# Kernel optimization log

Measured on AMD Instinct MI355X. Metric: run time of the kernel, lower is better.

The kernel has to match this reference:

```python
import jax, jax.numpy as jnp
import numpy as np


def _conv1x1(x, w, b):
    # x: [B, Cin, H, W], w: [Cout, Cin], b: [Cout]
    return jnp.einsum('bchw,oc->bohw', x, w) + b[None, :, None, None]


def setup_inputs() -> dict:
    key = jax.random.key(0)
    ks = jax.random.split(key, 9)
    B, C, H, W = 32, 512, 32, 32
    Cout, dn = 512, 512
    s_in = 1.0 / np.sqrt(C)
    s_out = 1.0 / np.sqrt(Cout)
    return {
        'x': jax.random.normal(ks[0], (B, C, H, W), jnp.float32),
        'wA': jax.random.uniform(ks[1], (Cout, C), jnp.float32, -s_in, s_in),
        'bA': jax.random.uniform(ks[2], (Cout,), jnp.float32, -s_in, s_in),
        'wB': jax.random.uniform(ks[3], (dn, C), jnp.float32, -s_in, s_in),
        'bB': jax.random.uniform(ks[4], (dn,), jnp.float32, -s_in, s_in),
        'wV': jax.random.uniform(ks[5], (dn, C), jnp.float32, -s_in, s_in),
        'bV': jax.random.uniform(ks[6], (dn,), jnp.float32, -s_in, s_in),
        'wR': jax.random.uniform(ks[7], (Cout, Cout), jnp.float32, -s_out, s_out),
        'bR': jax.random.uniform(ks[8], (Cout,), jnp.float32, -s_out, s_out),
    }


def reference(x, wA, bA, wB, bB, wV, bV, wR, bR):
    Bsz, C, H, W = x.shape
    Cout = wA.shape[0]
    A = _conv1x1(x, wA, bA).reshape(Bsz, Cout, H * W)          # [B, Cout, N]
    Bm = _conv1x1(x, wB, bB).reshape(Bsz, wB.shape[0], H * W)  # [B, dn, N]
    Vm = _conv1x1(x, wV, bV).reshape(Bsz, wV.shape[0], H * W)  # [B, dn, N]
    attn_maps = jax.nn.softmax(Bm, axis=-1)                    # softmax over spatial
    attn_vectors = jax.nn.softmax(Vm, axis=-1)                 # softmax over spatial
    glob_desc = jnp.einsum('bcn,bdn->bcd', A, attn_maps)       # [B, Cout, dn]
    Z = jnp.einsum('bcd,bdn->bcn', glob_desc, attn_vectors)    # [B, Cout, N]
    Z = Z.reshape(Bsz, Cout, H, W)
    Z = _conv1x1(Z, wR, bR)
    return Z
```

## Files before the change

### kernel.cpp

```cpp
#include <hip/hip_runtime.h>
#include <stdint.h>

typedef unsigned short u16;
typedef __bf16  bf16x8 __attribute__((ext_vector_type(8)));
typedef float   f32x4  __attribute__((ext_vector_type(4)));

__device__ __forceinline__ u16 f2bf(float f) {
    union { float f; unsigned u; } c; c.f = f;
    unsigned r = c.u + 0x7fffu + ((c.u >> 16) & 1u);
    return (u16)(r >> 16);
}
__device__ __forceinline__ float bf2f(u16 b) {
    union { unsigned u; float f; } c; c.u = ((unsigned)b) << 16; return c.f;
}

__device__ __forceinline__ void g2l16(const u16* g, u16* l) {
    __builtin_amdgcn_global_load_lds(
        (__attribute__((address_space(1))) void*)(uintptr_t)g,
        (__attribute__((address_space(3))) void*)(uint32_t)(uintptr_t)l,
        16, 0, 0);
}

template <int TM, bool HAS_BIAS, bool OUT_F32, bool EPI>
__device__ __forceinline__ void gemm_core(
    const u16* __restrict__ Ab, const u16* __restrict__ Bb, void* __restrict__ C,
    const float* __restrict__ bias, int N, int K, long cbase, int m0, int n0,
    const float* __restrict__ svec, const float* __restrict__ wRbA)
{
    constexpr int MI = TM / 32;
    constexpr int NA = TM / 32;
    __shared__ __align__(16) u16 As[TM * 64];
    __shared__ __align__(16) u16 Bs[128 * 64];

    const int t = threadIdx.x;
    const int w = t >> 6, lane = t & 63;
    const int wr = w >> 1, wc = w & 1;

    f32x4 acc[MI][4];
    const f32x4 zero = {0.f, 0.f, 0.f, 0.f};
#pragma unroll
    for (int i = 0; i < MI; ++i)
#pragma unroll
        for (int j = 0; j < 4; ++j) acc[i][j] = zero;

    int  aslot[NA]; long aoff[NA];
#pragma unroll
    for (int i = 0; i < NA; ++i) {
        const int s   = i * 256 + t;
        const int row = s >> 3;
        const int col = ((s & 7) ^ (row & 7)) * 8;
        aslot[i] = s * 8;
        aoff[i]  = (long)(m0 + row) * K + col;
    }
    int  bslot[4]; long boff[4];
#pragma unroll
    for (int i = 0; i < 4; ++i) {
        const int s   = i * 256 + t;
        const int row = s >> 3;
        const int col = ((s & 7) ^ (row & 7)) * 8;
        bslot[i] = s * 8;
        boff[i]  = (long)(n0 + row) * K + col;
    }

    const int fr = lane & 15;
    const int q  = lane >> 4;
    const int o0 = ((q ^ (fr & 7)) * 8);
    const u16* fa = &As[(wr * (TM / 2) + fr) * 64];
    const u16* fb = &Bs[(wc * 64 + fr) * 64];

    for (int k0 = 0; k0 < K; k0 += 64) {
#pragma unroll
        for (int i = 0; i < NA; ++i) g2l16(Ab + aoff[i] + k0, &As[aslot[i]]);
#pragma unroll
        for (int i = 0; i < 4; ++i)  g2l16(Bb + boff[i] + k0, &Bs[bslot[i]]);
        __syncthreads();

#pragma unroll
        for (int kh = 0; kh < 2; ++kh) {
            const int o = o0 ^ (kh * 32);
            bf16x8 af[MI], bv[4];
#pragma unroll
            for (int mi = 0; mi < MI; ++mi) af[mi] = *(const bf16x8*)(fa + mi * 1024 + o);
#pragma unroll
            for (int ni = 0; ni < 4; ++ni)  bv[ni] = *(const bf16x8*)(fb + ni * 1024 + o);
#pragma unroll
            for (int mi = 0; mi < MI; ++mi)
#pragma unroll
                for (int ni = 0; ni < 4; ++ni)
                    acc[mi][ni] = __builtin_amdgcn_mfma_f32_16x16x32_bf16(
                        af[mi], bv[ni], acc[mi][ni], 0, 0, 0);
        }
        __syncthreads();
    }

    const int ccol  = n0 + wc * 64 + fr;
    const int crow0 = m0 + wr * (TM / 2) + (lane >> 4) * 4;
    float se[4];
    if (EPI) {
#pragma unroll
        for (int ni = 0; ni < 4; ++ni) se[ni] = svec[ccol + ni * 16];
    }
#pragma unroll
    for (int mi = 0; mi < MI; ++mi) {
#pragma unroll
        for (int r = 0; r < 4; ++r) {
            const int row = crow0 + mi * 16 + r;
            float add = HAS_BIAS ? bias[row] : 0.f;
            float rk  = EPI ? wRbA[row] : 0.f;
#pragma unroll
            for (int ni = 0; ni < 4; ++ni) {
                float v = acc[mi][ni][r] + add;
                if (EPI) v += rk * se[ni];
                const long idx = cbase + (long)row * N + ccol + ni * 16;
                if (OUT_F32) ((float*)C)[idx] = v;
                else         ((u16*)C)[idx]   = f2bf(v);
            }
        }
    }
}

template <int TM, bool HAS_BIAS, bool OUT_F32>
__global__ __launch_bounds__(256) void gemm_nt(
    const u16* __restrict__ A, const u16* __restrict__ B, void* __restrict__ C,
    const float* __restrict__ bias, int N, int K, long sA, long sB, long sC)
{
    const int bz = blockIdx.z;
    gemm_core<TM, HAS_BIAS, OUT_F32, false>(
        A + (long)bz * sA, B + (long)bz * sB, C, bias, N, K,
        (long)bz * sC, blockIdx.y * TM, blockIdx.x * 128, nullptr, nullptr);
}

template <int TM, bool HAS_BIAS, bool OUT_F32, bool EPI>
__global__ __launch_bounds__(256) void gemm_nt_swz(
    const u16* __restrict__ A, const u16* __restrict__ B, void* __restrict__ C,
    const float* __restrict__ bias, int N, int K, long sA, long sB, long sC,
    int bxn, int bpb, const float* __restrict__ s_all,
    const float* __restrict__ wRbA)
{
    const int blk  = blockIdx.x;
    const int xcd  = blk & 7;
    const int slot = blk >> 3;
    const int b    = xcd + 8 * (slot / bpb);
    const int wi   = slot % bpb;
    const int bx   = wi % bxn;
    const int by   = wi / bxn;
    gemm_core<TM, HAS_BIAS, OUT_F32, EPI>(
        A + (long)b * sA, B + (long)b * sB, C, bias, N, K,
        (long)b * sC, by * TM, bx * 128,
        EPI ? s_all + (long)b * 1024 : nullptr, wRbA);
}

__global__ __launch_bounds__(512) void gemm2_y(
    const u16* __restrict__ A,
    const u16* __restrict__ B,
    u16* __restrict__ C,
    const float* __restrict__ bias)
{
    constexpr int K    = 512;
    constexpr int NT   = K / 32;
    constexpr int AREG = 256 * 32;
    constexpr int BUFQ = 2 * AREG;
    __shared__ __align__(16) u16 lds[4 * BUFQ];

    const int bz = blockIdx.z;
    const int m0 = blockIdx.y * 256;
    const int n0 = blockIdx.x * 256;
    const u16* Ab = A;
    const u16* Bb = B + (long)bz * (1024 * 512);
    u16*       Cb = C + (long)bz * ((long)1536 * 1024);

    const int t    = threadIdx.x;
    const int w    = t >> 6, lane = t & 63;
    const int wr   = w >> 2, wc = w & 3;
    const int fr   = lane & 15, q = lane >> 4;

    int  aslot[2]; long agoff[2], bgoff[2];
#pragma unroll
    for (int i = 0; i < 2; ++i) {
        const int ci  = i * 512 + t;
        const int row = ci >> 2;
        const int gc  = (ci & 3) ^ ((row >> 1) & 3);
        aslot[i] = ci * 8;
        agoff[i] = (long)(m0 + row) * K + gc * 8;
        bgoff[i] = (long)(n0 + row) * K + gc * 8;
    }

    const int rchunk = (q ^ ((fr >> 1) & 3)) * 8;
    const int abase  = (wr * 128 + fr) * 32 + rchunk;
    const int bbase  = (wc * 64  + fr) * 32 + rchunk;

    f32x4 acc[8][4];
    const f32x4 zero = {0.f, 0.f, 0.f, 0.f};
#pragma unroll
    for (int i = 0; i < 8; ++i)
#pragma unroll
        for (int j = 0; j < 4; ++j) acc[i][j] = zero;

#pragma unroll
    for (int i = 0; i < 2; ++i) g2l16(Ab + agoff[i],        &lds[aslot[i]]);
#pragma unroll
    for (int i = 0; i < 2; ++i) g2l16(Bb + bgoff[i],        &lds[AREG + aslot[i]]);
#pragma unroll
    for (int i = 0; i < 2; ++i) g2l16(Ab + agoff[i] + 32,   &lds[BUFQ + aslot[i]]);
#pragma unroll
    for (int i = 0; i < 2; ++i) g2l16(Bb + bgoff[i] + 32,   &lds[BUFQ + AREG + aslot[i]]);
    asm volatile("s_waitcnt vmcnt(4)" ::: "memory");
    __builtin_amdgcn_s_barrier();
    asm volatile("" ::: "memory");

#pragma unroll
    for (int kt = 0; kt < NT; ++kt) {
        const u16* Abuf = &lds[(kt & 3) * BUFQ];
        const u16* Bbuf = Abuf + AREG;
        u16* dst = &lds[((kt + 2) & 3) * BUFQ];
        const long kg = (long)(kt + 2) * 32;

        bf16x8 av[8], bv[4];
#pragma unroll
        for (int mi = 0; mi < 8; ++mi) av[mi] = *(const bf16x8*)(Abuf + abase + mi * 512);
#pragma unroll
        for (int ni = 0; ni < 4; ++ni) bv[ni] = *(const bf16x8*)(Bbuf + bbase + ni * 512);
        if (kt + 2 < NT) {
#pragma unroll
            for (int i = 0; i < 2; ++i) g2l16(Ab + agoff[i] + kg, dst + aslot[i]);
#pragma unroll
            for (int i = 0; i < 2; ++i) g2l16(Bb + bgoff[i] + kg, dst + AREG + aslot[i]);
        }
#pragma unroll
        for (int mi = 0; mi < 8; ++mi)
#pragma unroll
            for (int ni = 0; ni < 4; ++ni)
                acc[mi][ni] = __builtin_amdgcn_mfma_f32_16x16x32_bf16(
                    av[mi], bv[ni], acc[mi][ni], 0, 0, 0);

        if (kt + 1 < NT) {
            if (kt + 2 < NT) asm volatile("s_waitcnt vmcnt(4)" ::: "memory");
            else             asm volatile("s_waitcnt vmcnt(0)" ::: "memory");
            __builtin_amdgcn_s_barrier();
            asm volatile("" ::: "memory");
        }
    }

    const int ccol  = n0 + wc * 64 + fr;
    const int crow0 = m0 + wr * 128 + q * 4;
#pragma unroll
    for (int mi = 0; mi < 8; ++mi) {
#pragma unroll
        for (int r = 0; r < 4; ++r) {
            const int row = crow0 + mi * 16 + r;
            const float add = bias[row];
#pragma unroll
            for (int ni = 0; ni < 4; ++ni)
                Cb[(long)row * 1024 + ccol + ni * 16] = f2bf(acc[mi][ni][r] + add);
        }
    }
}

__global__ __launch_bounds__(256) void cast_transpose_x(
    const float* __restrict__ in, u16* __restrict__ out)
{
    __shared__ u16 tile[64][68];
    const int bz = blockIdx.z;
    const float* ip = in  + (long)bz * (512 * 1024);
    u16*         op = out + (long)bz * (1024 * 512);
    const int c0 = blockIdx.x * 64;
    const int r0 = blockIdx.y * 64;
    const int tx = threadIdx.x & 15;
    const int ty = threadIdx.x >> 4;
#pragma unroll
    for (int p = 0; p < 4; ++p) {
        const int row = ty + 16 * p;
        float4 v = *(const float4*)(ip + (long)(r0 + row) * 1024 + c0 + 4 * tx);
        ushort4 o;
        o.x = f2bf(v.x); o.y = f2bf(v.y); o.z = f2bf(v.z); o.w = f2bf(v.w);
        *(ushort4*)&tile[row][4 * tx] = o;
    }
    __syncthreads();
#pragma unroll
    for (int p = 0; p < 4; ++p) {
        const int orow = ty + 16 * p;
        ushort4 o;
        o.x = tile[4 * tx + 0][orow];
        o.y = tile[4 * tx + 1][orow];
        o.z = tile[4 * tx + 2][orow];
        o.w = tile[4 * tx + 3][orow];
        *(ushort4*)&op[(long)(c0 + orow) * 512 + r0 + 4 * tx] = o;
    }
}

__global__ __launch_bounds__(256) void transpose_colsum(
    const u16* __restrict__ in, u16* __restrict__ out, float* __restrict__ s,
    long sIn, long sOut)
{
    __shared__ u16 tile[64][68];
    const int bz = blockIdx.z;
    const u16* ip = in  + (long)bz * sIn;
    u16*       op = out + (long)bz * sOut;
    const int c0 = blockIdx.x * 64;
    const int r0 = blockIdx.y * 64;
    const int t  = threadIdx.x;
    const int tx = t & 15;
    const int ty = t >> 4;
#pragma unroll
    for (int p = 0; p < 4; ++p) {
        const int row = ty + 16 * p;
        ushort4 v = *(const ushort4*)(ip + (long)(r0 + row) * 1024 + c0 + 4 * tx);
        *(ushort4*)&tile[row][4 * tx] = v;
    }
    __syncthreads();
#pragma unroll
    for (int p = 0; p < 4; ++p) {
        const int orow = ty + 16 * p;
        ushort4 o;
        o.x = tile[4 * tx + 0][orow];
        o.y = tile[4 * tx + 1][orow];
        o.z = tile[4 * tx + 2][orow];
        o.w = tile[4 * tx + 3][orow];
        *(ushort4*)&op[(long)(c0 + orow) * 512 + r0 + 4 * tx] = o;
    }
    if (t < 64) {
        float a = 0.f;
#pragma unroll 8
        for (int d = 0; d < 64; ++d) a += bf2f(tile[d][t]);
        atomicAdd(&s[(long)bz * 1024 + c0 + t], a);
    }
}

__global__ __launch_bounds__(256) void cast_weights(
    const float* __restrict__ wA, const float* __restrict__ wB,
    const float* __restrict__ wV, const float* __restrict__ wR,
    const float* __restrict__ bB, const float* __restrict__ bV,
    u16* __restrict__ Wcat, u16* __restrict__ wRb, u16* __restrict__ wAtb,
    float* __restrict__ bcat)
{
    const int tid = blockIdx.x * 256 + threadIdx.x;
    if (tid < 262144) {
        Wcat[262144 + tid] = f2bf(wB[tid]);
    } else if (tid < 524288) {
        Wcat[262144 + tid] = f2bf(wV[tid - 262144]);
    } else if (tid < 786432) {
        wRb[tid - 524288] = f2bf(wR[tid - 524288]);
    } else if (tid < 1048576) {
        const int i = tid - 786432;
        wAtb[(i & 511) * 512 + (i >> 9)] = f2bf(wA[i]);
    } else if (tid < 1048576 + 1536) {
        const int j = tid - 1048576;
        bcat[j] = (j < 512) ? 0.f : (j < 1024) ? bB[j - 512] : bV[j - 1024];
    }
}

__global__ __launch_bounds__(256) void compute_wrba(
    const float* __restrict__ wR, const float* __restrict__ bA,
    float* __restrict__ wRbA)
{
    const int o    = blockIdx.x * 4 + (threadIdx.x >> 6);
    const int lane = threadIdx.x & 63;
    float a = 0.f;
#pragma unroll
    for (int c = lane; c < 512; c += 64) a += wR[o * 512 + c] * bA[c];
#pragma unroll
    for (int off = 32; off > 0; off >>= 1) a += __shfl_down(a, off);
    if (lane == 0) wRbA[o] = a;
}

__global__ __launch_bounds__(256) void softmax_rows(u16* __restrict__ Y)
{
    u16* row = Y + (long)blockIdx.y * (1536 * 1024) + (long)(512 + blockIdx.x) * 1024;
    const int t = threadIdx.x;
    ushort4 u = ((const ushort4*)row)[t];
    float v0 = bf2f(u.x), v1 = bf2f(u.y), v2 = bf2f(u.z), v3 = bf2f(u.w);

    float m = fmaxf(fmaxf(v0, v1), fmaxf(v2, v3));
#pragma unroll
    for (int off = 32; off > 0; off >>= 1) m = fmaxf(m, __shfl_down(m, off));

    __shared__ float smax[4];
    __shared__ float ssum[4];
    const int w = t >> 6, lane = t & 63;
    if (lane == 0) smax[w] = m;
    __syncthreads();
    m = fmaxf(fmaxf(smax[0], smax[1]), fmaxf(smax[2], smax[3]));

    float e0 = __expf(v0 - m), e1 = __expf(v1 - m);
    float e2 = __expf(v2 - m), e3 = __expf(v3 - m);
    float s = e0 + e1 + e2 + e3;
#pragma unroll
    for (int off = 32; off > 0; off >>= 1) s += __shfl_down(s, off);
    if (lane == 0) ssum[w] = s;
    __syncthreads();
    const float inv = 1.0f / (ssum[0] + ssum[1] + ssum[2] + ssum[3]);

    ushort4 o;
    o.x = f2bf(e0 * inv); o.y = f2bf(e1 * inv);
    o.z = f2bf(e2 * inv); o.w = f2bf(e3 * inv);
    ((ushort4*)row)[t] = o;
}

extern "C" void kernel_launch(void* const* d_in, const int* in_sizes, int n_in,
                              void* d_out, int out_size, void* d_ws, size_t ws_size,
                              hipStream_t stream)
{
    (void)in_sizes; (void)n_in; (void)out_size; (void)ws_size;
    const float* x  = (const float*)d_in[0];
    const float* wA = (const float*)d_in[1];
    const float* bA = (const float*)d_in[2];
    const float* wB = (const float*)d_in[3];
    const float* bB = (const float*)d_in[4];
    const float* wV = (const float*)d_in[5];
    const float* bV = (const float*)d_in[6];
    const float* wR = (const float*)d_in[7];
    const float* bR = (const float*)d_in[8];
    float* out = (float*)d_out;

    const int B = 32;
    const long sY = (long)1536 * 1024;

    char* p = (char*)d_ws;
    u16*   Y    = (u16*)p;   p += (long)B * sY * 2;
    u16*   H    = (u16*)p;   p += (long)B * 512 * 512 * 2;
    u16*   Wcat = (u16*)p;   p += (long)1536 * 512 * 2;
    u16*   wRb  = (u16*)p;   p += (long)512 * 512 * 2;
    u16*   wAtb = (u16*)p;   p += (long)512 * 512 * 2;
    float* bcat = (float*)p; p += 1536 * 4;
    float* svec = (float*)p; p += (long)B * 1024 * 4;
    float* wRbA = (float*)p; p += 512 * 4;

    u16* Xt = (u16*)d_out;
    u16* Vt = Y;

    cast_transpose_x<<<dim3(16, 8, B), 256, 0, stream>>>(x, Xt);
    cast_weights<<<dim3(4103), 256, 0, stream>>>(wA, wB, wV, wR, bB, bV,
                                                 Wcat, wRb, wAtb, bcat);
    compute_wrba<<<dim3(128), 256, 0, stream>>>(wR, bA, wRbA);
    hipMemsetAsync(svec, 0, (long)B * 1024 * 4, stream);

    gemm_nt<128, false, false><<<dim3(4, 4, 1), 256, 0, stream>>>(
        wRb, wAtb, Wcat, nullptr, 512, 512, 0, 0, 0);

    gemm2_y<<<dim3(4, 6, B), 512, 0, stream>>>(Wcat, Xt, Y, bcat);

    softmax_rows<<<dim3(1024, B), 256, 0, stream>>>(Y);

    gemm_nt_swz<128, false, false, false><<<dim3(512), 256, 0, stream>>>(
        Y, Y + (long)512 * 1024, H, nullptr, 512, 1024,
        sY, sY, (long)512 * 512, 4, 16, nullptr, nullptr);

    transpose_colsum<<<dim3(16, 8, B), 256, 0, stream>>>(
        Y + (long)1024 * 1024, Vt, svec, sY, sY);

    gemm_nt_swz<128, true, true, true><<<dim3(1024), 256, 0, stream>>>(
        H, Vt, out, bR, 1024, 512, (long)512 * 512, sY, (long)512 * 1024,
        8, 32, svec, wRbA);
}
```

Measured before the change: 308.9 us.

## Split softmax into stats pass and apply exp-normalize inside consumer loads

The softmax kernel no longer writes normalized rows back. It only stores each row's max and inverse sum. The attention GEMM and the transpose kernel then apply exp and scaling while loading the raw logits, which removes one write pass over the softmax region. gemm2_y also moves to a 1D grid with an XCD-aware block swizzle so blocks of the same batch share an L2. The cost is that the B operand no longer uses async global-to-LDS loads: it goes through registers and is exp'd per tile, recomputing exp for every M-tile that reads it.

```diff
diff --git a/kernel.cpp b/kernel.cpp
--- a/kernel.cpp
+++ b/kernel.cpp
@@ -4,6 +4,7 @@
 typedef unsigned short u16;
 typedef __bf16  bf16x8 __attribute__((ext_vector_type(8)));
 typedef float   f32x4  __attribute__((ext_vector_type(4)));
+typedef unsigned short us8 __attribute__((ext_vector_type(8)));
 
 __device__ __forceinline__ u16 f2bf(float f) {
     union { float f; unsigned u; } c; c.f = f;
@@ -21,11 +22,12 @@
         16, 0, 0);
 }
 
-template <int TM, bool HAS_BIAS, bool OUT_F32, bool EPI>
+template <int TM, bool HAS_BIAS, bool OUT_F32, bool EPI, bool SMAXB>
 __device__ __forceinline__ void gemm_core(
     const u16* __restrict__ Ab, const u16* __restrict__ Bb, void* __restrict__ C,
     const float* __restrict__ bias, int N, int K, long cbase, int m0, int n0,
-    const float* __restrict__ svec, const float* __restrict__ wRbA)
+    const float* __restrict__ svec, const float* __restrict__ wRbA,
+    const float2* __restrict__ bstats)
 {
     constexpr int MI = TM / 32;
     constexpr int NA = TM / 32;
@@ -53,6 +55,7 @@
         aoff[i]  = (long)(m0 + row) * K + col;
     }
     int  bslot[4]; long boff[4];
+    float2 bst[4];
 #pragma unroll
     for (int i = 0; i < 4; ++i) {
         const int s   = i * 256 + t;
@@ -60,6 +63,7 @@
         const int col = ((s & 7) ^ (row & 7)) * 8;
         bslot[i] = s * 8;
         boff[i]  = (long)(n0 + row) * K + col;
+        if (SMAXB) bst[i] = bstats[n0 + row];
     }
 
     const int fr = lane & 15;
@@ -71,8 +75,20 @@
     for (int k0 = 0; k0 < K; k0 += 64) {
 #pragma unroll
         for (int i = 0; i < NA; ++i) g2l16(Ab + aoff[i] + k0, &As[aslot[i]]);
-#pragma unroll
-        for (int i = 0; i < 4; ++i)  g2l16(Bb + boff[i] + k0, &Bs[bslot[i]]);
+        if (SMAXB) {
+#pragma unroll
+            for (int i = 0; i < 4; ++i) {
+                us8 raw = *(const us8*)(Bb + boff[i] + k0);
+                us8 o;
+#pragma unroll
+                for (int j = 0; j < 8; ++j)
+                    o[j] = f2bf(__expf(bf2f(raw[j]) - bst[i].x) * bst[i].y);
+                *(us8*)&Bs[bslot[i]] = o;
+            }
+        } else {
+#pragma unroll
+            for (int i = 0; i < 4; ++i) g2l16(Bb + boff[i] + k0, &Bs[bslot[i]]);
+        }
         __syncthreads();
 
 #pragma unroll
@@ -125,17 +141,17 @@
     const float* __restrict__ bias, int N, int K, long sA, long sB, long sC)
 {
     const int bz = blockIdx.z;
-    gemm_core<TM, HAS_BIAS, OUT_F32, false>(
+    gemm_core<TM, HAS_BIAS, OUT_F32, false, false>(
         A + (long)bz * sA, B + (long)bz * sB, C, bias, N, K,
-        (long)bz * sC, blockIdx.y * TM, blockIdx.x * 128, nullptr, nullptr);
-}
-
-template <int TM, bool HAS_BIAS, bool OUT_F32, bool EPI>
+        (long)bz * sC, blockIdx.y * TM, blockIdx.x * 128, nullptr, nullptr, nullptr);
+}
+
+template <int TM, bool HAS_BIAS, bool OUT_F32, bool EPI, bool SMAXB>
 __global__ __launch_bounds__(256) void gemm_nt_swz(
     const u16* __restrict__ A, const u16* __restrict__ B, void* __restrict__ C,
     const float* __restrict__ bias, int N, int K, long sA, long sB, long sC,
     int bxn, int bpb, const float* __restrict__ s_all,
-    const float* __restrict__ wRbA)
+    const float* __restrict__ wRbA, const float2* __restrict__ stats_all)
 {
     const int blk  = blockIdx.x;
     const int xcd  = blk & 7;
@@ -144,10 +160,11 @@
     const int wi   = slot % bpb;
     const int bx   = wi % bxn;
     const int by   = wi / bxn;
-    gemm_core<TM, HAS_BIAS, OUT_F32, EPI>(
+    gemm_core<TM, HAS_BIAS, OUT_F32, EPI, SMAXB>(
         A + (long)b * sA, B + (long)b * sB, C, bias, N, K,
         (long)b * sC, by * TM, bx * 128,
-        EPI ? s_all + (long)b * 1024 : nullptr, wRbA);
+        EPI ? s_all + (long)b * 1024 : nullptr, wRbA,
+        SMAXB ? stats_all + (long)b * 1024 : nullptr);
 }
 
 __global__ __launch_bounds__(512) void gemm2_y(
@@ -162,9 +179,14 @@
     constexpr int BUFQ = 2 * AREG;
     __shared__ __align__(16) u16 lds[4 * BUFQ];
 
-    const int bz = blockIdx.z;
-    const int m0 = blockIdx.y * 256;
-    const int n0 = blockIdx.x * 256;
+    const int blk  = blockIdx.x;
+    const int xcd  = blk & 7;
+    const int slot = blk >> 3;
+    const int bz   = xcd + 8 * (slot / 24);
+    const int wi   = slot % 24;
+    const int m0   = (wi >> 2) * 256;
+    const int n0   = (wi & 3) * 256;
+
     const u16* Ab = A;
     const u16* Bb = B + (long)bz * (1024 * 512);
     u16*       Cb = C + (long)bz * ((long)1536 * 1024);
@@ -290,7 +312,7 @@
 
 __global__ __launch_bounds__(256) void transpose_colsum(
     const u16* __restrict__ in, u16* __restrict__ out, float* __restrict__ s,
-    long sIn, long sOut)
+    long sIn, long sOut, const float2* __restrict__ stats_all)
 {
     __shared__ u16 tile[64][68];
     const int bz = blockIdx.z;
@@ -304,8 +326,14 @@
 #pragma unroll
     for (int p = 0; p < 4; ++p) {
         const int row = ty + 16 * p;
+        const float2 st = stats_all[(long)bz * 1024 + 512 + r0 + row];
         ushort4 v = *(const ushort4*)(ip + (long)(r0 + row) * 1024 + c0 + 4 * tx);
-        *(ushort4*)&tile[row][4 * tx] = v;
+        ushort4 o;
+        o.x = f2bf(__expf(bf2f(v.x) - st.x) * st.y);
+        o.y = f2bf(__expf(bf2f(v.y) - st.x) * st.y);
+        o.z = f2bf(__expf(bf2f(v.z) - st.x) * st.y);
+        o.w = f2bf(__expf(bf2f(v.w) - st.x) * st.y);
+        *(ushort4*)&tile[row][4 * tx] = o;
     }
     __syncthreads();
 #pragma unroll
@@ -363,9 +391,10 @@
     if (lane == 0) wRbA[o] = a;
 }
 
-__global__ __launch_bounds__(256) void softmax_rows(u16* __restrict__ Y)
-{
-    u16* row = Y + (long)blockIdx.y * (1536 * 1024) + (long)(512 + blockIdx.x) * 1024;
+__global__ __launch_bounds__(256) void softmax_stats(
+    const u16* __restrict__ Y, float2* __restrict__ stats)
+{
+    const u16* row = Y + (long)blockIdx.y * (1536 * 1024) + (long)(512 + blockIdx.x) * 1024;
     const int t = threadIdx.x;
     ushort4 u = ((const ushort4*)row)[t];
     float v0 = bf2f(u.x), v1 = bf2f(u.y), v2 = bf2f(u.z), v3 = bf2f(u.w);
@@ -388,12 +417,12 @@
     for (int off = 32; off > 0; off >>= 1) s += __shfl_down(s, off);
     if (lane == 0) ssum[w] = s;
     __syncthreads();
-    const float inv = 1.0f / (ssum[0] + ssum[1] + ssum[2] + ssum[3]);
-
-    ushort4 o;
-    o.x = f2bf(e0 * inv); o.y = f2bf(e1 * inv);
-    o.z = f2bf(e2 * inv); o.w = f2bf(e3 * inv);
-    ((ushort4*)row)[t] = o;
+    if (t == 0) {
+        float2 r;
+        r.x = m;
+        r.y = 1.0f / (ssum[0] + ssum[1] + ssum[2] + ssum[3]);
+        stats[(long)blockIdx.y * 1024 + blockIdx.x] = r;
+    }
 }
 
 extern "C" void kernel_launch(void* const* d_in, const int* in_sizes, int n_in,
@@ -424,6 +453,7 @@
     float* bcat = (float*)p; p += 1536 * 4;
     float* svec = (float*)p; p += (long)B * 1024 * 4;
     float* wRbA = (float*)p; p += 512 * 4;
+    float2* rowstats = (float2*)p; p += (long)B * 1024 * sizeof(float2);
 
     u16* Xt = (u16*)d_out;
     u16* Vt = Y;
@@ -437,18 +467,18 @@
     gemm_nt<128, false, false><<<dim3(4, 4, 1), 256, 0, stream>>>(
         wRb, wAtb, Wcat, nullptr, 512, 512, 0, 0, 0);
 
-    gemm2_y<<<dim3(4, 6, B), 512, 0, stream>>>(Wcat, Xt, Y, bcat);
-
-    softmax_rows<<<dim3(1024, B), 256, 0, stream>>>(Y);
-
-    gemm_nt_swz<128, false, false, false><<<dim3(512), 256, 0, stream>>>(
+    gemm2_y<<<dim3(768), 512, 0, stream>>>(Wcat, Xt, Y, bcat);
+
+    softmax_stats<<<dim3(1024, B), 256, 0, stream>>>(Y, rowstats);
+
+    gemm_nt_swz<128, false, false, false, true><<<dim3(512), 256, 0, stream>>>(
         Y, Y + (long)512 * 1024, H, nullptr, 512, 1024,
-        sY, sY, (long)512 * 512, 4, 16, nullptr, nullptr);
+        sY, sY, (long)512 * 512, 4, 16, nullptr, nullptr, rowstats);
 
     transpose_colsum<<<dim3(16, 8, B), 256, 0, stream>>>(
-        Y + (long)1024 * 1024, Vt, svec, sY, sY);
-
-    gemm_nt_swz<128, true, true, true><<<dim3(1024), 256, 0, stream>>>(
+        Y + (long)1024 * 1024, Vt, svec, sY, sY, rowstats);
+
+    gemm_nt_swz<128, true, true, true, false><<<dim3(1024), 256, 0, stream>>>(
         H, Vt, out, bR, 1024, 512, (long)512 * 512, sY, (long)512 * 1024,
-        8, 32, svec, wRbA);
-}
+        8, 32, svec, wRbA, nullptr);
+}
```

After: 311.8 us. Within noise of the previous version (+0.9%).

## Fuse V softmax into transpose, merge prep kernels, XCD-swizzle gemm2 grid

Applied to the files above, without the earlier changes.

For the V rows, the softmax kernel now writes only per-row max and inverse-sum statistics, and the transpose_colsum kernel applies exp and normalize as it loads. This removes one bf16 read/write pass over the V activations. The B-softmax output goes to a separate buffer inside the output region. Weight casting, the wR*bA product and the svec zeroing are merged into one launch, and gemm2_y uses a 1D grid that keeps each batch's tiles on one XCD for L2 reuse. The fused path rounds twice (bf16 logits, then bf16 probabilities), as the old path did, and it reuses d_out as scratch.

```diff
diff --git a/kernel.cpp b/kernel.cpp
--- a/kernel.cpp
+++ b/kernel.cpp
@@ -162,9 +162,14 @@
     constexpr int BUFQ = 2 * AREG;
     __shared__ __align__(16) u16 lds[4 * BUFQ];
 
-    const int bz = blockIdx.z;
-    const int m0 = blockIdx.y * 256;
-    const int n0 = blockIdx.x * 256;
+    const int blk  = blockIdx.x;
+    const int xcd  = blk & 7;
+    const int slot = blk >> 3;
+    const int bz   = xcd + 8 * (slot / 24);
+    const int wi   = slot % 24;
+    const int m0   = (wi >> 2) * 256;
+    const int n0   = (wi & 3) * 256;
+
     const u16* Ab = A;
     const u16* Bb = B + (long)bz * (1024 * 512);
     u16*       Cb = C + (long)bz * ((long)1536 * 1024);
@@ -290,7 +295,7 @@
 
 __global__ __launch_bounds__(256) void transpose_colsum(
     const u16* __restrict__ in, u16* __restrict__ out, float* __restrict__ s,
-    long sIn, long sOut)
+    long sIn, long sOut, const float2* __restrict__ stats_all)
 {
     __shared__ u16 tile[64][68];
     const int bz = blockIdx.z;
@@ -304,8 +309,14 @@
 #pragma unroll
     for (int p = 0; p < 4; ++p) {
         const int row = ty + 16 * p;
+        const float2 st = stats_all[(long)bz * 1024 + 512 + r0 + row];
         ushort4 v = *(const ushort4*)(ip + (long)(r0 + row) * 1024 + c0 + 4 * tx);
-        *(ushort4*)&tile[row][4 * tx] = v;
+        ushort4 o;
+        o.x = f2bf(__expf(bf2f(v.x) - st.x) * st.y);
+        o.y = f2bf(__expf(bf2f(v.y) - st.x) * st.y);
+        o.z = f2bf(__expf(bf2f(v.z) - st.x) * st.y);
+        o.w = f2bf(__expf(bf2f(v.w) - st.x) * st.y);
+        *(ushort4*)&tile[row][4 * tx] = o;
     }
     __syncthreads();
 #pragma unroll
@@ -326,46 +337,53 @@
     }
 }
 
-__global__ __launch_bounds__(256) void cast_weights(
+__global__ __launch_bounds__(256) void prep_weights(
     const float* __restrict__ wA, const float* __restrict__ wB,
     const float* __restrict__ wV, const float* __restrict__ wR,
-    const float* __restrict__ bB, const float* __restrict__ bV,
+    const float* __restrict__ bA, const float* __restrict__ bB,
+    const float* __restrict__ bV,
     u16* __restrict__ Wcat, u16* __restrict__ wRb, u16* __restrict__ wAtb,
-    float* __restrict__ bcat)
-{
-    const int tid = blockIdx.x * 256 + threadIdx.x;
-    if (tid < 262144) {
-        Wcat[262144 + tid] = f2bf(wB[tid]);
-    } else if (tid < 524288) {
-        Wcat[262144 + tid] = f2bf(wV[tid - 262144]);
-    } else if (tid < 786432) {
-        wRb[tid - 524288] = f2bf(wR[tid - 524288]);
-    } else if (tid < 1048576) {
-        const int i = tid - 786432;
-        wAtb[(i & 511) * 512 + (i >> 9)] = f2bf(wA[i]);
-    } else if (tid < 1048576 + 1536) {
-        const int j = tid - 1048576;
-        bcat[j] = (j < 512) ? 0.f : (j < 1024) ? bB[j - 512] : bV[j - 1024];
-    }
-}
-
-__global__ __launch_bounds__(256) void compute_wrba(
-    const float* __restrict__ wR, const float* __restrict__ bA,
-    float* __restrict__ wRbA)
-{
-    const int o    = blockIdx.x * 4 + (threadIdx.x >> 6);
-    const int lane = threadIdx.x & 63;
-    float a = 0.f;
-#pragma unroll
-    for (int c = lane; c < 512; c += 64) a += wR[o * 512 + c] * bA[c];
-#pragma unroll
-    for (int off = 32; off > 0; off >>= 1) a += __shfl_down(a, off);
-    if (lane == 0) wRbA[o] = a;
-}
-
-__global__ __launch_bounds__(256) void softmax_rows(u16* __restrict__ Y)
-{
-    u16* row = Y + (long)blockIdx.y * (1536 * 1024) + (long)(512 + blockIdx.x) * 1024;
+    float* __restrict__ bcat, float* __restrict__ wRbA,
+    float* __restrict__ svec)
+{
+    const int blk = blockIdx.x;
+    if (blk < 4103) {
+        const int tid = blk * 256 + threadIdx.x;
+        if (tid < 262144) {
+            Wcat[262144 + tid] = f2bf(wB[tid]);
+        } else if (tid < 524288) {
+            Wcat[262144 + tid] = f2bf(wV[tid - 262144]);
+        } else if (tid < 786432) {
+            wRb[tid - 524288] = f2bf(wR[tid - 524288]);
+        } else if (tid < 1048576) {
+            const int i = tid - 786432;
+            wAtb[(i & 511) * 512 + (i >> 9)] = f2bf(wA[i]);
+        } else if (tid < 1048576 + 1536) {
+            const int j = tid - 1048576;
+            bcat[j] = (j < 512) ? 0.f : (j < 1024) ? bB[j - 512] : bV[j - 1024];
+        }
+    } else if (blk < 4231) {
+        const int o    = (blk - 4103) * 4 + (threadIdx.x >> 6);
+        const int lane = threadIdx.x & 63;
+        float a = 0.f;
+#pragma unroll
+        for (int c = lane; c < 512; c += 64) a += wR[o * 512 + c] * bA[c];
+#pragma unroll
+        for (int off = 32; off > 0; off >>= 1) a += __shfl_down(a, off);
+        if (lane == 0) wRbA[o] = a;
+    } else {
+        const int idx = (blk - 4231) * 256 + threadIdx.x;
+        svec[idx] = 0.f;
+    }
+}
+
+__global__ __launch_bounds__(256) void softmax_apply(
+    const u16* __restrict__ Y, u16* __restrict__ attnM,
+    float2* __restrict__ stats)
+{
+    const int j  = blockIdx.x;
+    const int bz = blockIdx.y;
+    const u16* row = Y + (long)bz * (1536 * 1024) + (long)(512 + j) * 1024;
     const int t = threadIdx.x;
     ushort4 u = ((const ushort4*)row)[t];
     float v0 = bf2f(u.x), v1 = bf2f(u.y), v2 = bf2f(u.z), v3 = bf2f(u.w);
@@ -390,10 +408,15 @@
     __syncthreads();
     const float inv = 1.0f / (ssum[0] + ssum[1] + ssum[2] + ssum[3]);
 
-    ushort4 o;
-    o.x = f2bf(e0 * inv); o.y = f2bf(e1 * inv);
-    o.z = f2bf(e2 * inv); o.w = f2bf(e3 * inv);
-    ((ushort4*)row)[t] = o;
+    if (j < 512) {
+        ushort4 o;
+        o.x = f2bf(e0 * inv); o.y = f2bf(e1 * inv);
+        o.z = f2bf(e2 * inv); o.w = f2bf(e3 * inv);
+        ((ushort4*)(attnM + (long)bz * (512 * 1024) + (long)j * 1024))[t] = o;
+    } else if (t == 0) {
+        float2 r; r.x = m; r.y = inv;
+        stats[(long)bz * 1024 + j] = r;
+    }
 }
 
 extern "C" void kernel_launch(void* const* d_in, const int* in_sizes, int n_in,
@@ -424,29 +447,29 @@
     float* bcat = (float*)p; p += 1536 * 4;
     float* svec = (float*)p; p += (long)B * 1024 * 4;
     float* wRbA = (float*)p; p += 512 * 4;
-
-    u16* Xt = (u16*)d_out;
+    float2* rowstats = (float2*)p; p += (long)B * 1024 * sizeof(float2);
+
+    u16* Xt    = (u16*)d_out;
+    u16* attnM = (u16*)d_out + (long)16777216;
     u16* Vt = Y;
 
     cast_transpose_x<<<dim3(16, 8, B), 256, 0, stream>>>(x, Xt);
-    cast_weights<<<dim3(4103), 256, 0, stream>>>(wA, wB, wV, wR, bB, bV,
-                                                 Wcat, wRb, wAtb, bcat);
-    compute_wrba<<<dim3(128), 256, 0, stream>>>(wR, bA, wRbA);
-    hipMemsetAsync(svec, 0, (long)B * 1024 * 4, stream);
+    prep_weights<<<dim3(4359), 256, 0, stream>>>(wA, wB, wV, wR, bA, bB, bV,
+                                                 Wcat, wRb, wAtb, bcat, wRbA, svec);
 
     gemm_nt<128, false, false><<<dim3(4, 4, 1), 256, 0, stream>>>(
         wRb, wAtb, Wcat, nullptr, 512, 512, 0, 0, 0);
 
-    gemm2_y<<<dim3(4, 6, B), 512, 0, stream>>>(Wcat, Xt, Y, bcat);
-
-    softmax_rows<<<dim3(1024, B), 256, 0, stream>>>(Y);
+    gemm2_y<<<dim3(768), 512, 0, stream>>>(Wcat, Xt, Y, bcat);
+
+    softmax_apply<<<dim3(1024, B), 256, 0, stream>>>(Y, attnM, rowstats);
 
     gemm_nt_swz<128, false, false, false><<<dim3(512), 256, 0, stream>>>(
-        Y, Y + (long)512 * 1024, H, nullptr, 512, 1024,
-        sY, sY, (long)512 * 512, 4, 16, nullptr, nullptr);
+        Y, attnM, H, nullptr, 512, 1024,
+        sY, (long)512 * 1024, (long)512 * 512, 4, 16, nullptr, nullptr);
 
     transpose_colsum<<<dim3(16, 8, B), 256, 0, stream>>>(
-        Y + (long)1024 * 1024, Vt, svec, sY, sY);
+        Y + (long)1024 * 1024, Vt, svec, sY, sY, rowstats);
 
     gemm_nt_swz<128, true, true, true><<<dim3(1024), 256, 0, stream>>>(
         H, Vt, out, bR, 1024, 512, (long)512 * 512, sY, (long)512 * 1024,
```

Result: faster. 297.3 us (-3.8%).
